# Kernel tuning notes

Hardware: AMD Instinct MI355X
Metric: run time of the kernel (lower is better)

Reference implementation:

```python
import jax, jax.numpy as jnp
import numpy as np


def setup_inputs() -> dict:
    key = jax.random.key(0)
    ks = jax.random.split(key, 7)
    d, nq, nk = 64, 1024, 2048
    return {
        "query": jax.random.normal(ks[0], (1, d, nq), dtype=jnp.float32),
        "key": jax.random.normal(ks[1], (1, d, nk), dtype=jnp.float32),
        "value": jax.random.normal(ks[2], (1, d, nk), dtype=jnp.float32),
        # Conv1d(2d->d, k=1) weight squeezed to [d, 2d]; Conv1d(d->1, k=1) -> [1, d]
        "W1": jax.random.normal(ks[3], (d, 2 * d), dtype=jnp.float32) * (1.0 / np.sqrt(2 * d)),
        "b1": jax.random.normal(ks[4], (d,), dtype=jnp.float32) * 0.01,
        "W2": jax.random.normal(ks[5], (1, d), dtype=jnp.float32) * (1.0 / np.sqrt(d)),
        "b2": jax.random.normal(ks[6], (1,), dtype=jnp.float32) * 0.01,
    }


def reference(query, key, value, W1, b1, W2, b2):
    d = query.shape[1]
    # Split first conv weight into the query-half and key-half of the concat.
    # Conv1d with kernel 1 on cat([q_bcast, k_bcast]) == W1q @ q + W1k @ k (per pair).
    W1q, W1k = W1[:, :d], W1[:, d:]            # [h, d] each (h == d)
    qp = jnp.einsum('hd,bdq->bqh', W1q, query)  # [1, nq, h]
    kp = jnp.einsum('hd,bdk->bkh', W1k, key)    # [1, nk, h]
    # Pairwise hidden activations [1, nq, nk, h]
    h = jax.nn.relu(qp[:, :, None, :] + kp[:, None, :, :] + b1)
    scores = jnp.einsum('oh,bqkh->bqk', W2, h) + b2[0]  # [1, nq, nk]
    prob = jax.nn.softmax(scores, axis=-1)
    out = jnp.einsum('bnm,bdm->bdn', prob, value)        # [1, d, nq]
    return (out, scores)
```

## Files before the change

### kernel.cpp

```cpp
#include <hip/hip_runtime.h>


__global__ __launch_bounds__(256) void k1_proj(
    const float* __restrict__ q, const float* __restrict__ k,
    const float* __restrict__ W1, const float* __restrict__ b1,
    float* __restrict__ qp, float* __restrict__ kp)
{
  __shared__ float tile[256];
  const int t = threadIdx.x;
  const int b = blockIdx.x;
  if (b < 256) {
    const int nb = (b & 15) << 6;
    const int hb = (b >> 4) << 2;
    const int n = nb + (t & 63);
    const int h = hb + (t >> 6);
    const float* wr = W1 + h * 128;
    float acc = b1[h];
#pragma unroll
    for (int d = 0; d < 64; ++d) acc = fmaf(wr[d], q[(d << 10) + n], acc);
    tile[((t & 63) << 2) + (t >> 6)] = acc;
    __syncthreads();
    qp[((nb + (t >> 2)) << 6) + hb + (t & 3)] = tile[t];
  } else {
    const int b2 = b - 256;
    const int mb = (b2 & 31) << 6;
    const int hb = (b2 >> 5) << 2;
    const int m = mb + (t & 63);
    const int h = hb + (t >> 6);
    const float* wr = W1 + h * 128 + 64;
    float acc = 0.f;
#pragma unroll
    for (int d = 0; d < 64; ++d) acc = fmaf(wr[d], k[(d << 11) + m], acc);
    tile[((t & 63) << 2) + (t >> 6)] = acc;
    __syncthreads();
    kp[((mb + (t >> 2)) << 6) + hb + (t & 3)] = tile[t];
  }
}

__global__ __launch_bounds__(256, 2) void k2_scores(
    const float* __restrict__ qp, const float* __restrict__ kp,
    const float* __restrict__ W2, const float* __restrict__ b2p,
    float* __restrict__ scores, float* __restrict__ pbuf,
    float* __restrict__ lbuf)
{
  __shared__ float4 lds4[4096];
  const int t = threadIdx.x;
  const int lane = t & 63;
  const int wave = t >> 6;
  const int qt = blockIdx.x >> 2;
  const int ks = blockIdx.x & 3;
  const int q0 = (qt << 3) + (wave << 1);

  const float4* qp4 = (const float4*)(qp + (q0 << 6));
  float4 qa[16], qb[16];
#pragma unroll
  for (int i = 0; i < 16; ++i) { qa[i] = qp4[i]; qb[i] = qp4[16 + i]; }

  const float4* w24 = (const float4*)W2;
  const float b2v = b2p[0];
  const float4* kp4 = (const float4*)kp;
  const int sw = lane & 15;

  float lacc0 = 0.f, lacc1 = 0.f;

  for (int c = 0; c < 2; ++c) {
    const int kb = (ks << 9) + (c << 8);
    if (c) __syncthreads();
#pragma unroll
    for (int i = 0; i < 16; ++i) {
      const int idx = (i << 8) + t;
      const int row = idx >> 4;
      const int c4 = idx & 15;
      lds4[(row << 4) + (c4 ^ (row & 15))] = kp4[((kb + row) << 4) + c4];
    }
    __syncthreads();
    for (int s = 0; s < 4; ++s) {
      const int kl = (s << 6) + lane;
      float4 A0 = {0.f,0.f,0.f,0.f}, A1 = {0.f,0.f,0.f,0.f};
#pragma unroll
      for (int h4 = 0; h4 < 16; ++h4) {
        const float4 kf = lds4[(kl << 4) + (h4 ^ sw)];
        const float4 wv = w24[h4];
        A0.x = fmaf(wv.x, fmaxf(qa[h4].x + kf.x, 0.f), A0.x);
        A0.y = fmaf(wv.y, fmaxf(qa[h4].y + kf.y, 0.f), A0.y);
        A0.z = fmaf(wv.z, fmaxf(qa[h4].z + kf.z, 0.f), A0.z);
        A0.w = fmaf(wv.w, fmaxf(qa[h4].w + kf.w, 0.f), A0.w);
        A1.x = fmaf(wv.x, fmaxf(qb[h4].x + kf.x, 0.f), A1.x);
        A1.y = fmaf(wv.y, fmaxf(qb[h4].y + kf.y, 0.f), A1.y);
        A1.z = fmaf(wv.z, fmaxf(qb[h4].z + kf.z, 0.f), A1.z);
        A1.w = fmaf(wv.w, fmaxf(qb[h4].w + kf.w, 0.f), A1.w);
      }
      const float s0 = A0.x + A0.y + A0.z + A0.w + b2v;
      const float s1 = A1.x + A1.y + A1.z + A1.w + b2v;
      const int kg = kb + kl;
      scores[(q0 << 11) + kg] = s0;
      scores[((q0 + 1) << 11) + kg] = s1;
      const float e0 = __expf(s0);
      const float e1 = __expf(s1);
      pbuf[(q0 << 11) + kg] = e0;
      pbuf[((q0 + 1) << 11) + kg] = e1;
      lacc0 += e0; lacc1 += e1;
    }
  }
#pragma unroll
  for (int off = 32; off > 0; off >>= 1) {
    lacc0 += __shfl_xor(lacc0, off);
    lacc1 += __shfl_xor(lacc1, off);
  }
  if (lane == 0) {
    atomicAdd(&lbuf[q0], lacc0);
    atomicAdd(&lbuf[q0 + 1], lacc1);
  }
}

__global__ __launch_bounds__(256, 2) void k3_pv(
    const float* __restrict__ pbuf, const float* __restrict__ v,
    const float* __restrict__ lbuf, float* __restrict__ out)
{
  __shared__ float4 pS4[2048];
  __shared__ float vtS[8192];
  float4* vtS4w = (float4*)vtS;
  const float4* vtS4 = (const float4*)vtS;
  const int t = threadIdx.x;
  const int nt = blockIdx.x >> 4;
  const int ms = blockIdx.x & 15;
  const int n0b = nt << 6;
  const int mc4 = ms << 5;

  const float4* p4 = (const float4*)pbuf;
  const float4* v4 = (const float4*)v;
#pragma unroll
  for (int i = 0; i < 8; ++i) {
    const int idx = (i << 8) + t;
    const int n = idx >> 5, c = idx & 31;
    pS4[(n << 5) + (c ^ (n & 31))] = p4[((n0b + n) << 9) + mc4 + c];
  }
#pragma unroll
  for (int i = 0; i < 8; ++i) {
    const int idx = (i << 8) + t;
    const int d = idx >> 5, c = idx & 31;
    const float4 val = v4[(d << 9) + mc4 + c];
    const int m0 = c << 2;
    const int dc = d >> 2, dl = d & 3;
    vtS[((m0 + 0) << 6) + ((dc ^ ((m0 + 0) & 15)) << 2) + dl] = val.x;
    vtS[((m0 + 1) << 6) + ((dc ^ ((m0 + 1) & 15)) << 2) + dl] = val.y;
    vtS[((m0 + 2) << 6) + ((dc ^ ((m0 + 2) & 15)) << 2) + dl] = val.z;
    vtS[((m0 + 3) << 6) + ((dc ^ ((m0 + 3) & 15)) << 2) + dl] = val.w;
  }
  __syncthreads();

  const int tn = t >> 3;
  const int td = t & 7;
  const int td2 = td << 1;
  const int n0l = tn << 1, n1l = n0l + 1;
  const int sw0 = n0l & 31, sw1 = n1l & 31;

  float4 acc00 = {0,0,0,0}, acc01 = {0,0,0,0};
  float4 acc10 = {0,0,0,0}, acc11 = {0,0,0,0};

#define PV_STEP(AC) {                                          \
    const int swm = m & 15;                                    \
    const float4 b0 = vtS4[(m << 4) + (td2 ^ swm)];            \
    const float4 b1 = vtS4[(m << 4) + ((td2 + 1) ^ swm)];      \
    acc00.x = fmaf(a0.AC, b0.x, acc00.x);                      \
    acc00.y = fmaf(a0.AC, b0.y, acc00.y);                      \
    acc00.z = fmaf(a0.AC, b0.z, acc00.z);                      \
    acc00.w = fmaf(a0.AC, b0.w, acc00.w);                      \
    acc01.x = fmaf(a0.AC, b1.x, acc01.x);                      \
    acc01.y = fmaf(a0.AC, b1.y, acc01.y);                      \
    acc01.z = fmaf(a0.AC, b1.z, acc01.z);                      \
    acc01.w = fmaf(a0.AC, b1.w, acc01.w);                      \
    acc10.x = fmaf(a1.AC, b0.x, acc10.x);                      \
    acc10.y = fmaf(a1.AC, b0.y, acc10.y);                      \
    acc10.z = fmaf(a1.AC, b0.z, acc10.z);                      \
    acc10.w = fmaf(a1.AC, b0.w, acc10.w);                      \
    acc11.x = fmaf(a1.AC, b1.x, acc11.x);                      \
    acc11.y = fmaf(a1.AC, b1.y, acc11.y);                      \
    acc11.z = fmaf(a1.AC, b1.z, acc11.z);                      \
    acc11.w = fmaf(a1.AC, b1.w, acc11.w);                      \
    ++m; }

#pragma unroll 8
  for (int m4 = 0; m4 < 32; ++m4) {
    const float4 a0 = pS4[(n0l << 5) + (m4 ^ sw0)];
    const float4 a1 = pS4[(n1l << 5) + (m4 ^ sw1)];
    int m = m4 << 2;
    PV_STEP(x) PV_STEP(y) PV_STEP(z) PV_STEP(w)
  }
#undef PV_STEP

  const int n0 = n0b + n0l;
  const float i0 = 1.0f / lbuf[n0];
  const float i1 = 1.0f / lbuf[n0 + 1];
  const int dbase = td << 3;
  atomicAdd(&out[((dbase + 0) << 10) + n0], acc00.x * i0);
  atomicAdd(&out[((dbase + 1) << 10) + n0], acc00.y * i0);
  atomicAdd(&out[((dbase + 2) << 10) + n0], acc00.z * i0);
  atomicAdd(&out[((dbase + 3) << 10) + n0], acc00.w * i0);
  atomicAdd(&out[((dbase + 4) << 10) + n0], acc01.x * i0);
  atomicAdd(&out[((dbase + 5) << 10) + n0], acc01.y * i0);
  atomicAdd(&out[((dbase + 6) << 10) + n0], acc01.z * i0);
  atomicAdd(&out[((dbase + 7) << 10) + n0], acc01.w * i0);
  atomicAdd(&out[((dbase + 0) << 10) + n0 + 1], acc10.x * i1);
  atomicAdd(&out[((dbase + 1) << 10) + n0 + 1], acc10.y * i1);
  atomicAdd(&out[((dbase + 2) << 10) + n0 + 1], acc10.z * i1);
  atomicAdd(&out[((dbase + 3) << 10) + n0 + 1], acc10.w * i1);
  atomicAdd(&out[((dbase + 4) << 10) + n0 + 1], acc11.x * i1);
  atomicAdd(&out[((dbase + 5) << 10) + n0 + 1], acc11.y * i1);
  atomicAdd(&out[((dbase + 6) << 10) + n0 + 1], acc11.z * i1);
  atomicAdd(&out[((dbase + 7) << 10) + n0 + 1], acc11.w * i1);
}

extern "C" void kernel_launch(void* const* d_in, const int* in_sizes, int n_in,
                              void* d_out, int out_size, void* d_ws, size_t ws_size,
                              hipStream_t stream) {
  const float* query = (const float*)d_in[0];
  const float* key   = (const float*)d_in[1];
  const float* value = (const float*)d_in[2];
  const float* W1    = (const float*)d_in[3];
  const float* b1    = (const float*)d_in[4];
  const float* W2    = (const float*)d_in[5];
  const float* b2    = (const float*)d_in[6];

  float* out    = (float*)d_out;
  float* scores = out + 65536;

  float* ws = (float*)d_ws;
  float* qp = ws;
  float* kp = ws + 65536;
  float* pb = ws + 196608;
  float* lb = ws + 2293760;

  hipMemsetAsync(lb, 0, 1024 * sizeof(float), stream);
  hipMemsetAsync(out, 0, 65536 * sizeof(float), stream);
  k1_proj<<<768, 256, 0, stream>>>(query, key, W1, b1, qp, kp);
  k2_scores<<<512, 256, 0, stream>>>(qp, kp, W2, b2, scores, pb, lb);
  k3_pv<<<256, 256, 0, stream>>>(pb, value, lb, out);
}
```

Measured before the change: 110.9 us.

## Recompute exp in PV kernel, replace atomics with split-K partials plus reduce kernel

The scores kernel no longer writes a separate exp(scores) buffer. It stores per-split row-sum partials instead of using atomics. The PV kernel reads the scores directly, recomputes exp, uses a finer key split (32 slices of 64 keys) and writes partial outputs to a workspace. A new reduce kernel sums the partials, divides by the row sums and transposes into the output, which removes both memsets and the float atomics. The cost is an extra launch and 8 MB of partial writes and reads in exchange for dropping the 8 MB pbuf write and read.

```diff
diff --git a/kernel.cpp b/kernel.cpp
--- a/kernel.cpp
+++ b/kernel.cpp
@@ -40,8 +40,7 @@
 __global__ __launch_bounds__(256, 2) void k2_scores(
     const float* __restrict__ qp, const float* __restrict__ kp,
     const float* __restrict__ W2, const float* __restrict__ b2p,
-    float* __restrict__ scores, float* __restrict__ pbuf,
-    float* __restrict__ lbuf)
+    float* __restrict__ scores, float* __restrict__ lpart)
 {
   __shared__ float4 lds4[4096];
   const int t = threadIdx.x;
@@ -95,11 +94,8 @@
       const int kg = kb + kl;
       scores[(q0 << 11) + kg] = s0;
       scores[((q0 + 1) << 11) + kg] = s1;
-      const float e0 = __expf(s0);
-      const float e1 = __expf(s1);
-      pbuf[(q0 << 11) + kg] = e0;
-      pbuf[((q0 + 1) << 11) + kg] = e1;
-      lacc0 += e0; lacc1 += e1;
+      lacc0 += __expf(s0);
+      lacc1 += __expf(s1);
     }
   }
 #pragma unroll
@@ -108,60 +104,56 @@
     lacc1 += __shfl_xor(lacc1, off);
   }
   if (lane == 0) {
-    atomicAdd(&lbuf[q0], lacc0);
-    atomicAdd(&lbuf[q0 + 1], lacc1);
+    lpart[(ks << 10) + q0] = lacc0;
+    lpart[(ks << 10) + q0 + 1] = lacc1;
   }
 }
 
 __global__ __launch_bounds__(256, 2) void k3_pv(
-    const float* __restrict__ pbuf, const float* __restrict__ v,
-    const float* __restrict__ lbuf, float* __restrict__ out)
-{
-  __shared__ float4 pS4[2048];
-  __shared__ float vtS[8192];
-  float4* vtS4w = (float4*)vtS;
-  const float4* vtS4 = (const float4*)vtS;
-  const int t = threadIdx.x;
-  const int nt = blockIdx.x >> 4;
-  const int ms = blockIdx.x & 15;
+    const float* __restrict__ scores, const float* __restrict__ v,
+    float* __restrict__ part)
+{
+  __shared__ float4 pS4[1024];
+  __shared__ float4 vtS4[1024];
+  float* vtSf = (float*)vtS4;
+  const int t = threadIdx.x;
+  const int nt = blockIdx.x >> 5;
+  const int ms = blockIdx.x & 31;
   const int n0b = nt << 6;
-  const int mc4 = ms << 5;
-
-  const float4* p4 = (const float4*)pbuf;
+  const int mc4 = ms << 4;
+
+  const float4* s4 = (const float4*)scores;
   const float4* v4 = (const float4*)v;
 #pragma unroll
-  for (int i = 0; i < 8; ++i) {
+  for (int i = 0; i < 4; ++i) {
     const int idx = (i << 8) + t;
-    const int n = idx >> 5, c = idx & 31;
-    pS4[(n << 5) + (c ^ (n & 31))] = p4[((n0b + n) << 9) + mc4 + c];
-  }
-#pragma unroll
-  for (int i = 0; i < 8; ++i) {
+    const int n = idx >> 4, c = idx & 15;
+    float4 val = s4[((n0b + n) << 9) + mc4 + c];
+    val.x = __expf(val.x); val.y = __expf(val.y);
+    val.z = __expf(val.z); val.w = __expf(val.w);
+    pS4[(n << 4) + c] = val;
+  }
+#pragma unroll
+  for (int i = 0; i < 4; ++i) {
     const int idx = (i << 8) + t;
-    const int d = idx >> 5, c = idx & 31;
-    const float4 val = v4[(d << 9) + mc4 + c];
-    const int m0 = c << 2;
-    const int dc = d >> 2, dl = d & 3;
-    vtS[((m0 + 0) << 6) + ((dc ^ ((m0 + 0) & 15)) << 2) + dl] = val.x;
-    vtS[((m0 + 1) << 6) + ((dc ^ ((m0 + 1) & 15)) << 2) + dl] = val.y;
-    vtS[((m0 + 2) << 6) + ((dc ^ ((m0 + 2) & 15)) << 2) + dl] = val.z;
-    vtS[((m0 + 3) << 6) + ((dc ^ ((m0 + 3) & 15)) << 2) + dl] = val.w;
+    const int dd = idx >> 4, c = idx & 15;
+    const float4 val = v4[(dd << 9) + mc4 + c];
+    const int co = (((dd >> 2) ^ c) << 2) + (dd & 3);
+    vtSf[(c << 8) + co] = val.x;
+    vtSf[(c << 8) + 64 + co] = val.y;
+    vtSf[(c << 8) + 128 + co] = val.z;
+    vtSf[(c << 8) + 192 + co] = val.w;
   }
   __syncthreads();
 
-  const int tn = t >> 3;
-  const int td = t & 7;
-  const int td2 = td << 1;
+  const int tn = t >> 3, td = t & 7;
   const int n0l = tn << 1, n1l = n0l + 1;
-  const int sw0 = n0l & 31, sw1 = n1l & 31;
-
   float4 acc00 = {0,0,0,0}, acc01 = {0,0,0,0};
   float4 acc10 = {0,0,0,0}, acc11 = {0,0,0,0};
 
-#define PV_STEP(AC) {                                          \
-    const int swm = m & 15;                                    \
-    const float4 b0 = vtS4[(m << 4) + (td2 ^ swm)];            \
-    const float4 b1 = vtS4[(m << 4) + ((td2 + 1) ^ swm)];      \
+#define PV_STEP(J, AC) {                                       \
+    const float4 b0 = vtS4[(m4 << 6) + (J << 4) + c0];         \
+    const float4 b1 = vtS4[(m4 << 6) + (J << 4) + (c0 ^ 8)];   \
     acc00.x = fmaf(a0.AC, b0.x, acc00.x);                      \
     acc00.y = fmaf(a0.AC, b0.y, acc00.y);                      \
     acc00.z = fmaf(a0.AC, b0.z, acc00.z);                      \
@@ -178,37 +170,44 @@
     acc11.y = fmaf(a1.AC, b1.y, acc11.y);                      \
     acc11.z = fmaf(a1.AC, b1.z, acc11.z);                      \
     acc11.w = fmaf(a1.AC, b1.w, acc11.w);                      \
-    ++m; }
-
-#pragma unroll 8
-  for (int m4 = 0; m4 < 32; ++m4) {
-    const float4 a0 = pS4[(n0l << 5) + (m4 ^ sw0)];
-    const float4 a1 = pS4[(n1l << 5) + (m4 ^ sw1)];
-    int m = m4 << 2;
-    PV_STEP(x) PV_STEP(y) PV_STEP(z) PV_STEP(w)
+  }
+
+#pragma unroll
+  for (int m4 = 0; m4 < 16; ++m4) {
+    const float4 a0 = pS4[(n0l << 4) + m4];
+    const float4 a1 = pS4[(n1l << 4) + m4];
+    const int c0 = td ^ m4;
+    PV_STEP(0, x) PV_STEP(1, y) PV_STEP(2, z) PV_STEP(3, w)
   }
 #undef PV_STEP
 
-  const int n0 = n0b + n0l;
-  const float i0 = 1.0f / lbuf[n0];
-  const float i1 = 1.0f / lbuf[n0 + 1];
-  const int dbase = td << 3;
-  atomicAdd(&out[((dbase + 0) << 10) + n0], acc00.x * i0);
-  atomicAdd(&out[((dbase + 1) << 10) + n0], acc00.y * i0);
-  atomicAdd(&out[((dbase + 2) << 10) + n0], acc00.z * i0);
-  atomicAdd(&out[((dbase + 3) << 10) + n0], acc00.w * i0);
-  atomicAdd(&out[((dbase + 4) << 10) + n0], acc01.x * i0);
-  atomicAdd(&out[((dbase + 5) << 10) + n0], acc01.y * i0);
-  atomicAdd(&out[((dbase + 6) << 10) + n0], acc01.z * i0);
-  atomicAdd(&out[((dbase + 7) << 10) + n0], acc01.w * i0);
-  atomicAdd(&out[((dbase + 0) << 10) + n0 + 1], acc10.x * i1);
-  atomicAdd(&out[((dbase + 1) << 10) + n0 + 1], acc10.y * i1);
-  atomicAdd(&out[((dbase + 2) << 10) + n0 + 1], acc10.z * i1);
-  atomicAdd(&out[((dbase + 3) << 10) + n0 + 1], acc10.w * i1);
-  atomicAdd(&out[((dbase + 4) << 10) + n0 + 1], acc11.x * i1);
-  atomicAdd(&out[((dbase + 5) << 10) + n0 + 1], acc11.y * i1);
-  atomicAdd(&out[((dbase + 6) << 10) + n0 + 1], acc11.z * i1);
-  atomicAdd(&out[((dbase + 7) << 10) + n0 + 1], acc11.w * i1);
+  float4* part4 = (float4*)part;
+  const int pb0 = (ms << 14) + ((n0b + n0l) << 4);
+  const int pb1 = (ms << 14) + ((n0b + n1l) << 4);
+  part4[pb0 + td] = acc00;
+  part4[pb0 + td + 8] = acc01;
+  part4[pb1 + td] = acc10;
+  part4[pb1 + td + 8] = acc11;
+}
+
+__global__ __launch_bounds__(256) void k4_reduce(
+    const float* __restrict__ part, const float* __restrict__ lpart,
+    float* __restrict__ out)
+{
+  __shared__ float oS[256];
+  const int t = threadIdx.x;
+  const int nb = blockIdx.x << 2;
+  const int nl = t >> 6, d = t & 63;
+  const int n = nb + nl;
+  float sum = 0.f;
+#pragma unroll
+  for (int ms = 0; ms < 32; ++ms)
+    sum += part[(ms << 16) + (n << 6) + d];
+  const float l = lpart[n] + lpart[1024 + n] + lpart[2048 + n] + lpart[3072 + n];
+  oS[(nl << 6) + d] = sum / l;
+  __syncthreads();
+  const int d2 = t >> 2, n2 = t & 3;
+  out[(d2 << 10) + nb + n2] = oS[(n2 << 6) + d2];
 }
 
 extern "C" void kernel_launch(void* const* d_in, const int* in_sizes, int n_in,
@@ -225,15 +224,14 @@
   float* out    = (float*)d_out;
   float* scores = out + 65536;
 
-  float* ws = (float*)d_ws;
-  float* qp = ws;
-  float* kp = ws + 65536;
-  float* pb = ws + 196608;
-  float* lb = ws + 2293760;
-
-  hipMemsetAsync(lb, 0, 1024 * sizeof(float), stream);
-  hipMemsetAsync(out, 0, 65536 * sizeof(float), stream);
+  float* ws    = (float*)d_ws;
+  float* qp    = ws;
+  float* kp    = ws + 65536;
+  float* lpart = ws + 196608;
+  float* part  = ws + 200704;
+
   k1_proj<<<768, 256, 0, stream>>>(query, key, W1, b1, qp, kp);
-  k2_scores<<<512, 256, 0, stream>>>(qp, kp, W2, b2, scores, pb, lb);
-  k3_pv<<<256, 256, 0, stream>>>(pb, value, lb, out);
-}
+  k2_scores<<<512, 256, 0, stream>>>(qp, kp, W2, b2, scores, lpart);
+  k3_pv<<<512, 256, 0, stream>>>(scores, value, part);
+  k4_reduce<<<256, 256, 0, stream>>>(part, lpart, out);
+}
```

New measurement: 103.3 us. 1.07x faster.
